# Performance work log

Measured on AMD Instinct MI355X. Metric: run time of the kernel, lower is better.

Reference implementation:

```python
import jax, jax.numpy as jnp
import numpy as np

D_IN, D, BOX, REL, THR = 2048, 512, 8, 80, 0.5

def _ln(x, g, b):
    m = jnp.mean(x, -1, keepdims=True)
    v = jnp.mean((x - m) ** 2, -1, keepdims=True)
    return (x - m) * jax.lax.rsqrt(v + 1e-5) * g + b

def setup_inputs():
    key = jax.random.key(0)
    ks = jax.random.split(key, 24)
    B, N = 32, 50
    def lin(k, i, o):
        return jax.random.normal(k, (i, o), jnp.float32) / np.sqrt(i)
    z = lambda n: jnp.zeros((n,), jnp.float32)
    o = lambda n: jnp.ones((n,), jnp.float32)
    return {
        "images": jax.random.normal(ks[0], (B, N, D_IN), jnp.float32),
        "selfbbox": jax.random.uniform(ks[1], (B, N, BOX), jnp.float32),
        "bbox": jax.random.uniform(ks[2], (B, N, N, BOX), jnp.float32),
        "pre_w": lin(ks[3], D_IN, D), "pre_b": z(D), "pre_g": o(D), "pre_be": z(D),
        "subj_w": lin(ks[4], D, D), "subj_b": z(D),
        "obj_w": lin(ks[5], D, D), "obj_b": z(D),
        "ps1_w": lin(ks[6], BOX, 64), "ps1_b": z(64), "ps_g": o(64), "ps_be": z(64),
        "ps2_w": lin(ks[7], 64, 64), "ps2_b": z(64),
        "pr1_w": lin(ks[8], BOX, 64), "pr1_b": z(64), "pr_g": o(64), "pr_be": z(64),
        "pr2_w": lin(ks[9], 64, 64), "pr2_b": z(64),
        "rs_w": lin(ks[10], D + 64, 1), "rs_b": z(1),
        "rf_w": lin(ks[11], D + 64, REL), "rf_b": z(REL),
        "g1_w": lin(ks[12], D + REL, D + REL), "g1_b": z(D + REL),
        "g2_w": lin(ks[13], D + REL, D), "g2_b": z(D),
        "g3_w": lin(ks[14], D, D), "g3_b": z(D),
    }

def reference(images, selfbbox, bbox, pre_w, pre_b, pre_g, pre_be, subj_w, subj_b,
              obj_w, obj_b, ps1_w, ps1_b, ps_g, ps_be, ps2_w, ps2_b,
              pr1_w, pr1_b, pr_g, pr_be, pr2_w, pr2_b, rs_w, rs_b, rf_w, rf_b,
              g1_w, g1_b, g2_w, g2_b, g3_w, g3_b):
    B, N = images.shape[0], images.shape[1]
    mask = jnp.sum(images, -1) != 0.0                      # [B,N] valid nodes
    attention_mask = (~mask)[:, None, None, :]             # [B,1,1,N]
    mf = mask.astype(images.dtype)
    # preprocess: Linear -> ReLU -> (dropout=id at eval) -> LayerNorm
    x = _ln(jax.nn.relu(images @ pre_w + pre_b), pre_g, pre_be)  # [B,N,512]
    x_subj = jax.nn.relu(x @ subj_w + subj_b) * mf[..., None]
    x_obj = jax.nn.relu(x @ obj_w + obj_b) * mf[..., None]
    eye = jnp.eye(N, dtype=bool)
    # pairwise subject/object features: diag(i==j) holds subject, off-diag object j
    x_rela = jnp.where(eye[None, :, :, None], x_subj[:, :, None, :], x_obj[:, None, :, :])
    x_rela = x_rela * mf[:, :, None, None]
    # positional MLPs
    h = jax.nn.relu(selfbbox @ ps1_w + ps1_b)
    h = jax.nn.relu(_ln(h, ps_g, ps_be) @ ps2_w + ps2_b)
    pos_self = h * mf[..., None]
    h = jax.nn.relu(bbox @ pr1_w + pr1_b)
    h = jax.nn.relu(_ln(h, pr_g, pr_be) @ pr2_w + pr2_b)
    pos_relas = h * mf[:, None, :, None] * mf[:, :, None, None]
    pos_rela = jnp.where(eye[None, :, :, None], pos_self[:, :, None, :], pos_relas)
    pos_rela = pos_rela * mf[:, :, None, None]
    pair = jnp.concatenate([x_rela, pos_rela], axis=-1)    # [B,N,N,576]
    pair_mask = mask[:, :, None] & mask[:, None, :]        # [B,N,N]
    # Relationshipness: pairwise relatedness score p + attention-pooled relation feats
    logits = (pair @ rs_w + rs_b)[..., 0]                  # [B,N,N]
    p = jax.nn.sigmoid(logits) * pair_mask.astype(images.dtype)
    attn = jax.nn.softmax(jnp.where(pair_mask, logits, -1e9), axis=2)
    feat = jax.nn.relu(pair @ rf_w + rf_b)                 # [B,N,N,80]
    relas = jnp.einsum('bij,bijf->bif', attn, feat) * mf[..., None]
    xx = jnp.concatenate([x, relas], axis=-1)              # [B,N,592]
    # dynamic edge threshold -> block-diagonal graph, expressed densely per image
    A = p > THR                                            # edge i->j
    Ahat = A | eye[None]                                   # add remaining self loops
    Af = Ahat.astype(xx.dtype)
    deg = jnp.sum(Af, axis=1)                              # in-degree at target j (>=1)
    dinv = jax.lax.rsqrt(deg)
    An = Af * dinv[:, :, None] * dinv[:, None, :]          # sym-normalized adjacency
    def gcn(hh, w, b):
        return jnp.einsum('bij,bif->bjf', An, hh @ w) + b
    x1 = jax.nn.relu(gcn(xx, g1_w, g1_b))
    x2 = jax.nn.relu(gcn(x1, g2_w, g2_b))
    x3 = jax.nn.relu(gcn(x2, g3_w, g3_b))
    outs = jnp.concatenate([x[:, None], x3[:, None]], axis=1)  # [B,2,N,512]
    return (outs, attention_mask)
```

## Files before the change

kernel.cpp:

```cpp
#include <hip/hip_runtime.h>
#include <hip/hip_bf16.h>

typedef __hip_bfloat16 bf16;

#define BB 32
#define NN 50
#define DIN 2048
#define DD 512
#define PD 64
#define FF 80
#define GG 592
#define BN (BB*NN)

#define O_FLAG  0
#define O_MF    16
#define O_SS    1616
#define O_SO    3216
#define O_PS    4816
#define O_FS    107216
#define O_FO    235216
#define O_RL    363216
#define O_LG    491216
#define O_AN    571216
#define O_T     651216
#define O_X1    1598416
#define O_X2    2545616
#define O_WPRE  3364816
#define O_BPRE  4413392
#define O_GPRE  4413904
#define O_EPRE  4414416
#define O_WSUBJ 4414928
#define O_BSUBJ 4677072
#define O_WOBJ  4677584
#define O_BOBJ  4939728
#define O_WPS1  4940240
#define O_BPS1  4940752
#define O_GPS   4940816
#define O_EPS   4940880
#define O_WPS2  4940944
#define O_BPS2  4945040
#define O_WPR1  4945104
#define O_BPR1  4945616
#define O_GPR   4945680
#define O_EPR   4945744
#define O_WPR2  4945808
#define O_BPR2  4949904
#define O_WRS   4949968
#define O_BRS   4950544
#define O_WRF   4950560
#define O_BRF   4996640
#define O_WG1   4996736
#define O_BG1   5347200
#define O_WG2   5347792
#define O_BG2   5650896
#define O_WG3   5651408
#define O_BG3   5913552
#define O_FT    5914064

#define PSLICE  819200

__device__ __forceinline__ float b2f(bf16 x){ return __bfloat162float(x); }

__device__ __forceinline__ float LDI(const bf16* p, size_t i, int f32m){
    if(f32m){
        bf16 a=p[2*i], b=p[2*i+1];
        unsigned short lo,hi;
        __builtin_memcpy(&lo,&a,2); __builtin_memcpy(&hi,&b,2);
        unsigned v=((unsigned)hi<<16)|(unsigned)lo;
        float f; __builtin_memcpy(&f,&v,4);
        return f;
    }
    return __bfloat162float(p[i]);
}

__global__ void k_flag(const bf16* __restrict__ images, float* __restrict__ ws){
    __shared__ int cnt;
    if(threadIdx.x==0) cnt=0;
    __syncthreads();
    bf16 h=images[2*threadIdx.x];
    unsigned short u; __builtin_memcpy(&u,&h,2);
    unsigned e=(u>>7)&0xFF;
    int sane=((u&0x7FFF)==0 || (e>=0x70&&e<=0x85))?1:0;
    atomicAdd(&cnt,sane);
    __syncthreads();
    if(threadIdx.x==0) ws[O_FLAG]=(cnt<48)?1.f:0.f;
}

__device__ __forceinline__ void conv(const bf16* s, float* d, int n, int F, int i0, int st){
    for(int g=i0; g<n; g+=st) d[g]=LDI(s,(size_t)g,F);
}
__global__ void kw(const bf16* p0,const bf16* p1,const bf16* p2,const bf16* p3,
                   const bf16* p4,const bf16* p5,const bf16* p6,const bf16* p7,
                   const bf16* p8,const bf16* p9,const bf16* p10,const bf16* p11,
                   const bf16* p12,const bf16* p13,const bf16* p14,const bf16* p15,
                   const bf16* p16,const bf16* p17,const bf16* p18,const bf16* p19,
                   const bf16* p20,const bf16* p21,const bf16* p22,const bf16* p23,
                   const bf16* p24,const bf16* p25,const bf16* p26,const bf16* p27,
                   const bf16* p28,const bf16* p29, float* __restrict__ ws){
    int F=ws[O_FLAG]>0.5f;
    int i0=blockIdx.x*256+threadIdx.x, st=gridDim.x*256;
    conv(p0, ws+O_WPRE, 1048576,F,i0,st);
    conv(p1, ws+O_BPRE, 512,F,i0,st);
    conv(p2, ws+O_GPRE, 512,F,i0,st);
    conv(p3, ws+O_EPRE, 512,F,i0,st);
    conv(p4, ws+O_WSUBJ,262144,F,i0,st);
    conv(p5, ws+O_BSUBJ,512,F,i0,st);
    conv(p6, ws+O_WOBJ, 262144,F,i0,st);
    conv(p7, ws+O_BOBJ, 512,F,i0,st);
    conv(p8, ws+O_WPS1, 512,F,i0,st);
    conv(p9, ws+O_BPS1, 64,F,i0,st);
    conv(p10,ws+O_GPS,  64,F,i0,st);
    conv(p11,ws+O_EPS,  64,F,i0,st);
    conv(p12,ws+O_WPS2, 4096,F,i0,st);
    conv(p13,ws+O_BPS2, 64,F,i0,st);
    conv(p14,ws+O_WPR1, 512,F,i0,st);
    conv(p15,ws+O_BPR1, 64,F,i0,st);
    conv(p16,ws+O_GPR,  64,F,i0,st);
    conv(p17,ws+O_EPR,  64,F,i0,st);
    conv(p18,ws+O_WPR2, 4096,F,i0,st);
    conv(p19,ws+O_BPR2, 64,F,i0,st);
    conv(p20,ws+O_WRS,  576,F,i0,st);
    conv(p21,ws+O_BRS,  1,F,i0,st);
    conv(p22,ws+O_WRF,  46080,F,i0,st);
    conv(p23,ws+O_BRF,  80,F,i0,st);
    conv(p24,ws+O_WG1,  350464,F,i0,st);
    conv(p25,ws+O_BG1,  592,F,i0,st);
    conv(p26,ws+O_WG2,  303104,F,i0,st);
    conv(p27,ws+O_BG2,  512,F,i0,st);
    conv(p28,ws+O_WG3,  262144,F,i0,st);
    conv(p29,ws+O_BG3,  512,F,i0,st);
}

__global__ void k_mask(const bf16* __restrict__ images, float* __restrict__ ws,
                       float* __restrict__ out){
    int t=threadIdx.x, wv=t>>6, ln=t&63;
    int r=blockIdx.x*4+wv;
    int F=ws[O_FLAG]>0.5f;
    float s=0.f;
    for(int k=ln;k<DIN;k+=64) s+=LDI(images,(size_t)r*DIN+k,F);
    for(int m=32;m>0;m>>=1) s+=__shfl_xor(s,m,64);
    if(ln==0){
        float mf=(s!=0.f)?1.f:0.f;
        ws[O_MF+r]=mf;
        out[(size_t)BB*2*NN*DD+r]=1.f-mf;
    }
}

__global__ void __launch_bounds__(256,4) k_x(const bf16* __restrict__ images,
                                             float* __restrict__ ws){
    __shared__ float as[8*256];
    int blk=blockIdx.x, t=threadIdx.x;
    int rg=blk>>3, ks=blk&7;
    int r0=rg*8, kbase=ks*256;
    int F=ws[O_FLAG]>0.5f;
    for(int idx=t; idx<8*256; idx+=256){
        int row=idx>>8, k=idx&255;
        as[idx]=LDI(images,(size_t)(r0+row)*DIN+kbase+k,F);
    }
    __syncthreads();
    const float* wP=ws+O_WPRE+(size_t)kbase*DD;
    int c0=t, c1=t+256;
    float acc[8][2]={};
    for(int k0=0;k0<256;k0+=8){
        float w0[8],w1[8];
        #pragma unroll
        for(int u=0;u<8;u++){ w0[u]=wP[(size_t)(k0+u)*DD+c0]; w1[u]=wP[(size_t)(k0+u)*DD+c1]; }
        #pragma unroll
        for(int u=0;u<8;u++){
            #pragma unroll
            for(int row=0;row<8;row++){
                float v=as[row*256+k0+u];
                acc[row][0]+=v*w0[u]; acc[row][1]+=v*w1[u];
            }
        }
    }
    float* P=ws + ((ks<7)? (O_FT+(size_t)ks*PSLICE) : (size_t)O_T);
    #pragma unroll
    for(int row=0;row<8;row++){
        size_t b=(size_t)(r0+row)*DD;
        P[b+c0]=acc[row][0]; P[b+c1]=acc[row][1];
    }
}

__global__ void __launch_bounds__(256,4) k_xr(float* __restrict__ ws, float* __restrict__ out){
    __shared__ float red[256];
    int blk=blockIdx.x, t=threadIdx.x;
    int r0=blk*4;
    const float* bPre=ws+O_BPRE; const float* gPre=ws+O_GPRE; const float* ePre=ws+O_EPRE;
    int c0=t, c1=t+256;
    for(int row=0;row<4;row++){
        int r=r0+row;
        float y0=bPre[c0], y1=bPre[c1];
        for(int ks=0;ks<8;ks++){
            const float* P=ws + ((ks<7)? (O_FT+(size_t)ks*PSLICE) : (size_t)O_T);
            y0+=P[(size_t)r*DD+c0]; y1+=P[(size_t)r*DD+c1];
        }
        y0=fmaxf(y0,0.f); y1=fmaxf(y1,0.f);
        red[t]=y0+y1; __syncthreads();
        for(int o=128;o>0;o>>=1){ if(t<o) red[t]+=red[t+o]; __syncthreads(); }
        float mean=red[0]/DD; __syncthreads();
        float d0=y0-mean, d1=y1-mean;
        red[t]=d0*d0+d1*d1; __syncthreads();
        for(int o=128;o>0;o>>=1){ if(t<o) red[t]+=red[t+o]; __syncthreads(); }
        float rstd=rsqrtf(red[0]/DD+1e-5f);
        __syncthreads();
        float xv0=d0*rstd*gPre[c0]+ePre[c0];
        float xv1=d1*rstd*gPre[c1]+ePre[c1];
        size_t ob=((size_t)(r/NN)*2)*NN*DD+(size_t)(r%NN)*DD;
        out[ob+c0]=xv0; out[ob+c1]=xv1;
    }
}

__global__ void __launch_bounds__(256,4) k_so(const float* __restrict__ out,
                                              float* __restrict__ ws){
    __shared__ float xs[4*DD];
    __shared__ float ys[4*DD];
    __shared__ float mrow_s[4];
    int blk=blockIdx.x, t=threadIdx.x;
    int rg=blk>>1, mat=blk&1;
    int r0=rg*4;
    for(int idx=t; idx<4*DD; idx+=256){
        int row=idx>>9, k=idx&511;
        int r=r0+row;
        xs[idx]=out[((size_t)(r/NN)*2)*NN*DD+(size_t)(r%NN)*DD+k];
    }
    if(t<4) mrow_s[t]=ws[O_MF+r0+t];
    __syncthreads();
    const float* W =ws+(mat?O_WOBJ:O_WSUBJ);
    const float* Bb=ws+(mat?O_BOBJ:O_BSUBJ);
    int c0=t, c1=t+256;
    float acc[4][2]={};
    for(int k0=0;k0<DD;k0+=8){
        float w0[8],w1[8];
        #pragma unroll
        for(int u=0;u<8;u++){ w0[u]=W[(size_t)(k0+u)*DD+c0]; w1[u]=W[(size_t)(k0+u)*DD+c1]; }
        #pragma unroll
        for(int u=0;u<8;u++){
            #pragma unroll
            for(int row=0;row<4;row++){
                float v=xs[row*DD+k0+u];
                acc[row][0]+=v*w0[u]; acc[row][1]+=v*w1[u];
            }
        }
    }
    #pragma unroll
    for(int row=0;row<4;row++){
        ys[row*DD+c0]=fmaxf(acc[row][0]+Bb[c0],0.f)*mrow_s[row];
        ys[row*DD+c1]=fmaxf(acc[row][1]+Bb[c1],0.f)*mrow_s[row];
    }
    __syncthreads();
    int wv=t>>6, ln=t&63;
    const float* wRs=ws+O_WRS;
    float ps=0.f;
    for(int k=ln;k<DD;k+=64) ps+=ys[wv*DD+k]*wRs[k];
    for(int m=32;m>0;m>>=1) ps+=__shfl_xor(ps,m,64);
    if(ln==0) ws[(mat?O_SO:O_SS)+r0+wv]=ps;
    const float* wRf=ws+O_WRF;
    for(int pass=0;pass<2;pass++){
        if(t<160){
            int row=pass*2+t/80, f=t%80;
            const float* xv=ys+row*DD;
            float a=0.f;
            for(int k=0;k<DD;k++) a+=xv[k]*wRf[(size_t)k*FF+f];
            ws[(mat?O_FO:O_FS)+(size_t)(r0+row)*FF+f]=a;
        }
    }
}

__global__ void k_pos_self(const bf16* __restrict__ sb, float* __restrict__ ws){
    __shared__ float h[PD];
    __shared__ float stat[2];
    int r=blockIdx.x, t=threadIdx.x;
    int F=ws[O_FLAG]>0.5f;
    const float* w1=ws+O_WPS1;
    float acc=0.f;
    for(int q=0;q<8;q++) acc+=LDI(sb,(size_t)r*8+q,F)*w1[q*PD+t];
    acc=fmaxf(acc+ws[O_BPS1+t],0.f);
    h[t]=acc; __syncthreads();
    if(t==0){
        float sm=0; for(int k=0;k<PD;k++) sm+=h[k];
        float mean=sm/PD;
        float v=0; for(int k=0;k<PD;k++){float d=h[k]-mean; v+=d*d;}
        stat[0]=mean; stat[1]=rsqrtf(v/PD+1e-5f);
    }
    __syncthreads();
    float hn=(acc-stat[0])*stat[1]*ws[O_GPS+t]+ws[O_EPS+t];
    h[t]=hn; __syncthreads();
    float a2=0.f;
    const float* w2=ws+O_WPS2;
    for(int k=0;k<PD;k++) a2+=h[k]*w2[k*PD+t];
    ws[O_PS+(size_t)r*PD+t]=fmaxf(a2+ws[O_BPS2+t],0.f)*ws[O_MF+r];
}

#define PSTRIDE 68

__global__ void __launch_bounds__(256,2) k_pair(const bf16* __restrict__ bbox,
                                                float* __restrict__ ws){
    __shared__ float W2t[64*PSTRIDE];
    __shared__ float WrfT[80*PSTRIDE];
    __shared__ float zb[64*PSTRIDE];
    __shared__ float pv[64*PSTRIDE];
    __shared__ float w1s[512];
    __shared__ float b1s[64], g1s[64], be1s[64], b2s[64], wrss[64];
    __shared__ float brfs[80];
    __shared__ float bbs[512];
    __shared__ float rowmi[64], rowmj[64], rowbase[64];
    __shared__ int   rowfb[64], rowps[64], rowdg[64];

    int t=threadIdx.x;
    int blk=blockIdx.x;
    int F=ws[O_FLAG]>0.5f;
    float rsb=ws[O_BRS];

    for(int idx=t; idx<4096; idx+=256){ int k=idx>>6, c=idx&63; W2t[k*PSTRIDE+c]=ws[O_WPR2+idx]; }
    for(int idx=t; idx<5120; idx+=256){
        int k=idx/80, f=idx-k*80;
        WrfT[f*PSTRIDE+k]=ws[O_WRF+(size_t)(512+k)*FF+f];
    }
    for(int idx=t; idx<512; idx+=256) w1s[idx]=ws[O_WPR1+idx];
    for(int idx=t; idx<512; idx+=256) bbs[idx]=LDI(bbox,(size_t)blk*512+idx,F);
    if(t<64){
        b1s[t]=ws[O_BPR1+t]; g1s[t]=ws[O_GPR+t]; be1s[t]=ws[O_EPR+t];
        b2s[t]=ws[O_BPR2+t]; wrss[t]=ws[O_WRS+512+t];
    } else if(t<144){
        brfs[t-64]=ws[O_BRF+t-64];
    }
    if(t<64){
        int p=blk*64+t;
        int r=p/NN, j=p-r*NN;
        int b=r/NN, i=r-b*NN;
        int dg=(i==j);
        rowmi[t]=ws[O_MF+r];
        rowmj[t]=ws[O_MF+b*NN+j];
        rowdg[t]=dg;
        rowbase[t]=dg? ws[O_SS+r] : ws[O_SO+b*NN+j];
        rowfb[t]=dg? (O_FS+r*FF) : (O_FO+(b*NN+j)*FF);
        rowps[t]=O_PS+r*PD;
    }
    __syncthreads();

    int wv=t>>6, ln=t&63;
    for(int q=0;q<16;q++){
        int m=wv*16+q;
        float acc=0.f;
        #pragma unroll
        for(int u=0;u<8;u++) acc+=bbs[m*8+u]*w1s[u*64+ln];
        float h1=fmaxf(acc+b1s[ln],0.f);
        float sm=h1;
        for(int o=32;o>0;o>>=1) sm+=__shfl_xor(sm,o,64);
        float mean=sm*(1.f/64.f);
        float d=h1-mean;
        float vv=d*d;
        for(int o=32;o>0;o>>=1) vv+=__shfl_xor(vv,o,64);
        float rstd=rsqrtf(vv*(1.f/64.f)+1e-5f);
        zb[m*PSTRIDE+ln]=d*rstd*g1s[ln]+be1s[ln];
    }
    __syncthreads();

    int tr=t>>4, tc=t&15;
    int m0=tr*4, c0=tc*4;
    {
        float a1[4][4]={};
        for(int k0=0;k0<64;k0+=4){
            float4 zv[4], wvv[4];
            #pragma unroll
            for(int i=0;i<4;i++) zv[i]=*(const float4*)&zb[(m0+i)*PSTRIDE+k0];
            #pragma unroll
            for(int u=0;u<4;u++) wvv[u]=*(const float4*)&W2t[(k0+u)*PSTRIDE+c0];
            #pragma unroll
            for(int i=0;i<4;i++){
                const float* zp=(const float*)&zv[i];
                #pragma unroll
                for(int u=0;u<4;u++){
                    const float* wp=(const float*)&wvv[u];
                    float zk=zp[u];
                    a1[i][0]+=zk*wp[0]; a1[i][1]+=zk*wp[1];
                    a1[i][2]+=zk*wp[2]; a1[i][3]+=zk*wp[3];
                }
            }
        }
        #pragma unroll
        for(int i=0;i<4;i++){
            int m=m0+i;
            float sc=rowmi[m]*rowmj[m];
            float4 o;
            o.x=fmaxf(a1[i][0]+b2s[c0+0],0.f)*sc;
            o.y=fmaxf(a1[i][1]+b2s[c0+1],0.f)*sc;
            o.z=fmaxf(a1[i][2]+b2s[c0+2],0.f)*sc;
            o.w=fmaxf(a1[i][3]+b2s[c0+3],0.f)*sc;
            *(float4*)&pv[m*PSTRIDE+c0]=o;
        }
    }
    __syncthreads();

    for(int idx=t; idx<4096; idx+=256){
        int m=idx>>6, c=idx&63;
        if(rowdg[m]) pv[m*PSTRIDE+c]=ws[rowps[m]+c];
    }
    __syncthreads();

    for(int q=0;q<16;q++){
        int m=wv*16+q;
        float lp=pv[m*PSTRIDE+ln]*wrss[ln];
        for(int o=32;o>0;o>>=1) lp+=__shfl_xor(lp,o,64);
        if(ln==0){
            int p=blk*64+m;
            ws[O_LG+p]=rowmi[m]*rowbase[m]+lp+rsb;
        }
    }

    {
        int c5=tc*5;
        float a2[4][5]={};
        for(int k0=0;k0<64;k0+=4){
            float4 zv[4], wv5[5];
            #pragma unroll
            for(int i=0;i<4;i++) zv[i]=*(const float4*)&pv[(m0+i)*PSTRIDE+k0];
            #pragma unroll
            for(int j=0;j<5;j++) wv5[j]=*(const float4*)&WrfT[(c5+j)*PSTRIDE+k0];
            #pragma unroll
            for(int i=0;i<4;i++){
                const float* zp=(const float*)&zv[i];
                #pragma unroll
                for(int j=0;j<5;j++){
                    const float* wp=(const float*)&wv5[j];
                    a2[i][j]+=zp[0]*wp[0]+zp[1]*wp[1]+zp[2]*wp[2]+zp[3]*wp[3];
                }
            }
        }
        #pragma unroll
        for(int i=0;i<4;i++){
            int m=m0+i;
            int p=blk*64+m;
            float mi=rowmi[m];
            const float* fb=ws+rowfb[m];
            #pragma unroll
            for(int j=0;j<5;j++){
                int c=c5+j;
                ws[O_FT+(size_t)p*FF+c]=fmaxf(mi*fb[c]+a2[i][j]+brfs[c],0.f);
            }
        }
    }
}

__global__ void k_relas(float* __restrict__ ws){
    __shared__ float attn[NN];
    int r=blockIdx.x, t=threadIdx.x;
    int b=r/NN;
    float mi=ws[O_MF+r];
    if(t<NN){
        float mj=ws[O_MF+b*NN+t];
        bool pm=(mi>0.5f)&&(mj>0.5f);
        attn[t]=pm? ws[O_LG+(size_t)r*NN+t] : -1e9f;
    }
    __syncthreads();
    if(t==0){
        float mx=-1e30f;
        for(int j=0;j<NN;j++) mx=fmaxf(mx,attn[j]);
        float sm=0.f;
        for(int j=0;j<NN;j++){ float e=__expf(attn[j]-mx); attn[j]=e; sm+=e; }
        float inv=1.f/sm;
        for(int j=0;j<NN;j++) attn[j]*=inv;
    }
    __syncthreads();
    if(t<FF){
        float s=0.f;
        const float* ft=ws+O_FT+(size_t)r*NN*FF;
        for(int j=0;j<NN;j++) s+=attn[j]*ft[(size_t)j*FF+t];
        ws[O_RL+(size_t)r*FF+t]=s*mi;
    }
}

__global__ void k_adj(float* __restrict__ ws){
    __shared__ float Af[NN*NN];
    __shared__ float dinv[NN];
    int b=blockIdx.x, t=threadIdx.x;
    for(int idx=t; idx<NN*NN; idx+=256){
        int i=idx/NN, j=idx%NN;
        float l=ws[O_LG+(size_t)b*NN*NN+idx];
        bool a=(l>0.f)&&(ws[O_MF+b*NN+i]>0.5f)&&(ws[O_MF+b*NN+j]>0.5f);
        Af[idx]=(a||i==j)?1.f:0.f;
    }
    __syncthreads();
    if(t<NN){
        float dg=0.f;
        for(int i=0;i<NN;i++) dg+=Af[i*NN+t];
        dinv[t]=rsqrtf(dg);
    }
    __syncthreads();
    for(int idx=t; idx<NN*NN; idx+=256){
        int i=idx/NN, j=idx%NN;
        ws[O_AN+(size_t)b*NN*NN+idx]=Af[idx]*dinv[i]*dinv[j];
    }
}

__global__ void kt(int mode, const float* __restrict__ out, const float* __restrict__ ws,
                   const float* __restrict__ W, float* __restrict__ T,
                   int K, int NCOL, int NTILE){
    __shared__ float xs[10*GG];
    int blk=blockIdx.x, t=threadIdx.x;
    int rg=blk/NTILE, tile=blk%NTILE;
    for(int idx=t; idx<10*K; idx+=256){
        int row=idx/K, k=idx-row*K;
        int gr=rg*10+row;
        float v;
        if(mode==0){
            int bb=gr/NN, ii=gr-bb*NN;
            if(k<DD) v=out[(size_t)(2*bb)*NN*DD+(size_t)ii*DD+k];
            else     v=ws[O_RL+(size_t)gr*FF+(k-DD)];
        } else if(mode==1) v=ws[O_X1+(size_t)gr*GG+k];
        else               v=ws[O_X2+(size_t)gr*DD+k];
        xs[row*K+k]=v;
    }
    __syncthreads();
    int c=tile*256+t;
    if(c>=NCOL) return;
    float acc[10];
    #pragma unroll
    for(int u=0;u<10;u++) acc[u]=0.f;
    for(int k=0;k<K;k++){
        float w=W[(size_t)k*NCOL+c];
        #pragma unroll
        for(int u=0;u<10;u++) acc[u]+=xs[u*K+k]*w;
    }
    int gr0=rg*10;
    #pragma unroll
    for(int u=0;u<10;u++) T[(size_t)(gr0+u)*NCOL+c]=acc[u];
}

__global__ void ka(int mode, float* __restrict__ ws, const float* __restrict__ bias,
                   float* __restrict__ out, int NCOL){
    __shared__ float acol[NN];
    int rj=blockIdx.x, t=threadIdx.x;
    int b=rj/NN, j=rj-b*NN;
    if(t<NN) acol[t]=ws[O_AN+(size_t)b*NN*NN+t*NN+j];
    __syncthreads();
    const float* Tb=ws+O_T+(size_t)b*NN*NCOL;
    for(int c=t;c<NCOL;c+=256){
        float acc=0.f;
        for(int i2=0;i2<NN;i2++) acc+=acol[i2]*Tb[(size_t)i2*NCOL+c];
        float v=fmaxf(acc+bias[c],0.f);
        if(mode==2)      out[(size_t)(2*b+1)*NN*DD+(size_t)j*DD+c]=v;
        else if(mode==1) ws[O_X2+(size_t)rj*DD+c]=v;
        else             ws[O_X1+(size_t)rj*GG+c]=v;
    }
}

extern "C" void kernel_launch(void* const* d_in, const int* in_sizes, int n_in,
                              void* d_out, int out_size, void* d_ws, size_t ws_size,
                              hipStream_t stream) {
    const bf16* images  = (const bf16*)d_in[0];
    const bf16* selfbbox= (const bf16*)d_in[1];
    const bf16* bbox    = (const bf16*)d_in[2];

    float* out=(float*)d_out;
    float* ws =(float*)d_ws;

    k_flag<<<1,64,0,stream>>>(images, ws);
    kw<<<512,256,0,stream>>>((const bf16*)d_in[3],(const bf16*)d_in[4],(const bf16*)d_in[5],
                             (const bf16*)d_in[6],(const bf16*)d_in[7],(const bf16*)d_in[8],
                             (const bf16*)d_in[9],(const bf16*)d_in[10],(const bf16*)d_in[11],
                             (const bf16*)d_in[12],(const bf16*)d_in[13],(const bf16*)d_in[14],
                             (const bf16*)d_in[15],(const bf16*)d_in[16],(const bf16*)d_in[17],
                             (const bf16*)d_in[18],(const bf16*)d_in[19],(const bf16*)d_in[20],
                             (const bf16*)d_in[21],(const bf16*)d_in[22],(const bf16*)d_in[23],
                             (const bf16*)d_in[24],(const bf16*)d_in[25],(const bf16*)d_in[26],
                             (const bf16*)d_in[27],(const bf16*)d_in[28],(const bf16*)d_in[29],
                             (const bf16*)d_in[30],(const bf16*)d_in[31],(const bf16*)d_in[32],
                             ws);
    k_mask<<<400,256,0,stream>>>(images, ws, out);
    k_x<<<1600,256,0,stream>>>(images, ws);
    k_xr<<<400,256,0,stream>>>(ws, out);
    k_pos_self<<<BN,PD,0,stream>>>(selfbbox, ws);
    k_so<<<800,256,0,stream>>>(out, ws);
    k_pair<<<1250,256,0,stream>>>(bbox, ws);
    k_relas<<<BN,128,0,stream>>>(ws);
    k_adj<<<BB,256,0,stream>>>(ws);

    kt<<<160*3,256,0,stream>>>(0, out, ws, ws+O_WG1, ws+O_T, GG, GG, 3);
    ka<<<BN,256,0,stream>>>(0, ws, ws+O_BG1, out, GG);
    kt<<<160*2,256,0,stream>>>(1, out, ws, ws+O_WG2, ws+O_T, GG, DD, 2);
    ka<<<BN,256,0,stream>>>(1, ws, ws+O_BG2, out, DD);
    kt<<<160*2,256,0,stream>>>(2, out, ws, ws+O_WG3, ws+O_T, DD, DD, 2);
    ka<<<BN,256,0,stream>>>(2, ws, ws+O_BG3, out, DD);
}
```

Before: 666.6 us.

## Double pair tile per block, reuse shared buffers, and warp-shuffle softmax

```diff
diff --git a/kernel.cpp b/kernel.cpp
--- a/kernel.cpp
+++ b/kernel.cpp
@@ -293,40 +293,43 @@
 }
 
 #define PSTRIDE 68
+#define ZROW(m) ((m)*PSTRIDE + (((m)>>3)<<2))
 
 __global__ void __launch_bounds__(256,2) k_pair(const bf16* __restrict__ bbox,
                                                 float* __restrict__ ws){
-    __shared__ float W2t[64*PSTRIDE];
-    __shared__ float WrfT[80*PSTRIDE];
-    __shared__ float zb[64*PSTRIDE];
-    __shared__ float pv[64*PSTRIDE];
+    __shared__ float zp[128*PSTRIDE+64];
+    __shared__ float wbuf[80*PSTRIDE];
     __shared__ float w1s[512];
+    __shared__ float bbs[1024];
     __shared__ float b1s[64], g1s[64], be1s[64], b2s[64], wrss[64];
     __shared__ float brfs[80];
-    __shared__ float bbs[512];
-    __shared__ float rowmi[64], rowmj[64], rowbase[64];
-    __shared__ int   rowfb[64], rowps[64], rowdg[64];
+    __shared__ float rowmi[128], rowmj[128], rowbase[128];
+    __shared__ int   rowfb[128], rowps[128], rowdg[128];
 
     int t=threadIdx.x;
     int blk=blockIdx.x;
     int F=ws[O_FLAG]>0.5f;
     float rsb=ws[O_BRS];
 
-    for(int idx=t; idx<4096; idx+=256){ int k=idx>>6, c=idx&63; W2t[k*PSTRIDE+c]=ws[O_WPR2+idx]; }
-    for(int idx=t; idx<5120; idx+=256){
-        int k=idx/80, f=idx-k*80;
-        WrfT[f*PSTRIDE+k]=ws[O_WRF+(size_t)(512+k)*FF+f];
-    }
+    float wrfreg[20];
+    #pragma unroll
+    for(int u=0;u<20;u++){
+        int idx=t+256*u;
+        int f=idx>>6, k=idx&63;
+        wrfreg[u]=ws[O_WRF+(size_t)(512+k)*FF+f];
+    }
+
+    for(int idx=t; idx<4096; idx+=256){ int k=idx>>6, c=idx&63; wbuf[k*PSTRIDE+c]=ws[O_WPR2+idx]; }
     for(int idx=t; idx<512; idx+=256) w1s[idx]=ws[O_WPR1+idx];
-    for(int idx=t; idx<512; idx+=256) bbs[idx]=LDI(bbox,(size_t)blk*512+idx,F);
+    for(int idx=t; idx<1024; idx+=256) bbs[idx]=LDI(bbox,(size_t)blk*1024+idx,F);
     if(t<64){
         b1s[t]=ws[O_BPR1+t]; g1s[t]=ws[O_GPR+t]; be1s[t]=ws[O_EPR+t];
         b2s[t]=ws[O_BPR2+t]; wrss[t]=ws[O_WRS+512+t];
     } else if(t<144){
         brfs[t-64]=ws[O_BRF+t-64];
     }
-    if(t<64){
-        int p=blk*64+t;
+    if(t<128){
+        int p=blk*128+t;
         int r=p/NN, j=p-r*NN;
         int b=r/NN, i=r-b*NN;
         int dg=(i==j);
@@ -340,8 +343,8 @@
     __syncthreads();
 
     int wv=t>>6, ln=t&63;
-    for(int q=0;q<16;q++){
-        int m=wv*16+q;
+    for(int q=0;q<32;q++){
+        int m=wv*32+q;
         float acc=0.f;
         #pragma unroll
         for(int u=0;u<8;u++) acc+=bbs[m*8+u]*w1s[u*64+ln];
@@ -353,114 +356,117 @@
         float vv=d*d;
         for(int o=32;o>0;o>>=1) vv+=__shfl_xor(vv,o,64);
         float rstd=rsqrtf(vv*(1.f/64.f)+1e-5f);
-        zb[m*PSTRIDE+ln]=d*rstd*g1s[ln]+be1s[ln];
+        zp[ZROW(m)+ln]=d*rstd*g1s[ln]+be1s[ln];
     }
     __syncthreads();
 
     int tr=t>>4, tc=t&15;
-    int m0=tr*4, c0=tc*4;
-    {
-        float a1[4][4]={};
-        for(int k0=0;k0<64;k0+=4){
-            float4 zv[4], wvv[4];
-            #pragma unroll
-            for(int i=0;i<4;i++) zv[i]=*(const float4*)&zb[(m0+i)*PSTRIDE+k0];
-            #pragma unroll
-            for(int u=0;u<4;u++) wvv[u]=*(const float4*)&W2t[(k0+u)*PSTRIDE+c0];
-            #pragma unroll
-            for(int i=0;i<4;i++){
-                const float* zp=(const float*)&zv[i];
-                #pragma unroll
-                for(int u=0;u<4;u++){
-                    const float* wp=(const float*)&wvv[u];
-                    float zk=zp[u];
-                    a1[i][0]+=zk*wp[0]; a1[i][1]+=zk*wp[1];
-                    a1[i][2]+=zk*wp[2]; a1[i][3]+=zk*wp[3];
-                }
+    int m0=tr*8, c0=tc*4;
+    float a1[8][4]={};
+    for(int k0=0;k0<64;k0+=4){
+        float4 zv[8], wvv[4];
+        #pragma unroll
+        for(int i=0;i<8;i++) zv[i]=*(const float4*)&zp[ZROW(m0+i)+k0];
+        #pragma unroll
+        for(int u=0;u<4;u++) wvv[u]=*(const float4*)&wbuf[(k0+u)*PSTRIDE+c0];
+        #pragma unroll
+        for(int i=0;i<8;i++){
+            const float* zpp=(const float*)&zv[i];
+            #pragma unroll
+            for(int u=0;u<4;u++){
+                const float* wp=(const float*)&wvv[u];
+                float zk=zpp[u];
+                a1[i][0]+=zk*wp[0]; a1[i][1]+=zk*wp[1];
+                a1[i][2]+=zk*wp[2]; a1[i][3]+=zk*wp[3];
             }
         }
-        #pragma unroll
-        for(int i=0;i<4;i++){
-            int m=m0+i;
+    }
+    __syncthreads();
+
+    #pragma unroll
+    for(int i=0;i<8;i++){
+        int m=m0+i;
+        float4 o;
+        if(rowdg[m]){
+            const float* ps=ws+rowps[m];
+            o.x=ps[c0]; o.y=ps[c0+1]; o.z=ps[c0+2]; o.w=ps[c0+3];
+        } else {
             float sc=rowmi[m]*rowmj[m];
-            float4 o;
             o.x=fmaxf(a1[i][0]+b2s[c0+0],0.f)*sc;
             o.y=fmaxf(a1[i][1]+b2s[c0+1],0.f)*sc;
             o.z=fmaxf(a1[i][2]+b2s[c0+2],0.f)*sc;
             o.w=fmaxf(a1[i][3]+b2s[c0+3],0.f)*sc;
-            *(float4*)&pv[m*PSTRIDE+c0]=o;
-        }
-    }
-    __syncthreads();
-
-    for(int idx=t; idx<4096; idx+=256){
-        int m=idx>>6, c=idx&63;
-        if(rowdg[m]) pv[m*PSTRIDE+c]=ws[rowps[m]+c];
-    }
-    __syncthreads();
-
-    for(int q=0;q<16;q++){
-        int m=wv*16+q;
-        float lp=pv[m*PSTRIDE+ln]*wrss[ln];
+        }
+        *(float4*)&zp[ZROW(m)+c0]=o;
+    }
+    #pragma unroll
+    for(int u=0;u<20;u++){
+        int idx=t+256*u;
+        wbuf[(idx>>6)*PSTRIDE+(idx&63)]=wrfreg[u];
+    }
+    __syncthreads();
+
+    for(int q=0;q<32;q++){
+        int m=wv*32+q;
+        float lp=zp[ZROW(m)+ln]*wrss[ln];
         for(int o=32;o>0;o>>=1) lp+=__shfl_xor(lp,o,64);
         if(ln==0){
-            int p=blk*64+m;
-            ws[O_LG+p]=rowmi[m]*rowbase[m]+lp+rsb;
+            ws[O_LG+(size_t)blk*128+m]=rowmi[m]*rowbase[m]+lp+rsb;
         }
     }
 
     {
         int c5=tc*5;
-        float a2[4][5]={};
+        float a2[8][5]={};
         for(int k0=0;k0<64;k0+=4){
-            float4 zv[4], wv5[5];
-            #pragma unroll
-            for(int i=0;i<4;i++) zv[i]=*(const float4*)&pv[(m0+i)*PSTRIDE+k0];
-            #pragma unroll
-            for(int j=0;j<5;j++) wv5[j]=*(const float4*)&WrfT[(c5+j)*PSTRIDE+k0];
-            #pragma unroll
-            for(int i=0;i<4;i++){
-                const float* zp=(const float*)&zv[i];
+            float4 zv[8], wv5[5];
+            #pragma unroll
+            for(int i=0;i<8;i++) zv[i]=*(const float4*)&zp[ZROW(m0+i)+k0];
+            #pragma unroll
+            for(int j=0;j<5;j++) wv5[j]=*(const float4*)&wbuf[(c5+j)*PSTRIDE+k0];
+            #pragma unroll
+            for(int i=0;i<8;i++){
+                const float* zpp=(const float*)&zv[i];
                 #pragma unroll
                 for(int j=0;j<5;j++){
                     const float* wp=(const float*)&wv5[j];
-                    a2[i][j]+=zp[0]*wp[0]+zp[1]*wp[1]+zp[2]*wp[2]+zp[3]*wp[3];
+                    a2[i][j]+=zpp[0]*wp[0]+zpp[1]*wp[1]+zpp[2]*wp[2]+zpp[3]*wp[3];
                 }
             }
         }
         #pragma unroll
-        for(int i=0;i<4;i++){
+        for(int i=0;i<8;i++){
             int m=m0+i;
-            int p=blk*64+m;
+            size_t p=(size_t)blk*128+m;
             float mi=rowmi[m];
             const float* fb=ws+rowfb[m];
             #pragma unroll
             for(int j=0;j<5;j++){
                 int c=c5+j;
-                ws[O_FT+(size_t)p*FF+c]=fmaxf(mi*fb[c]+a2[i][j]+brfs[c],0.f);
+                ws[O_FT+p*FF+c]=fmaxf(mi*fb[c]+a2[i][j]+brfs[c],0.f);
             }
         }
     }
 }
 
 __global__ void k_relas(float* __restrict__ ws){
-    __shared__ float attn[NN];
+    __shared__ float attn[64];
     int r=blockIdx.x, t=threadIdx.x;
     int b=r/NN;
     float mi=ws[O_MF+r];
-    if(t<NN){
-        float mj=ws[O_MF+b*NN+t];
-        bool pm=(mi>0.5f)&&(mj>0.5f);
-        attn[t]=pm? ws[O_LG+(size_t)r*NN+t] : -1e9f;
-    }
-    __syncthreads();
-    if(t==0){
-        float mx=-1e30f;
-        for(int j=0;j<NN;j++) mx=fmaxf(mx,attn[j]);
-        float sm=0.f;
-        for(int j=0;j<NN;j++){ float e=__expf(attn[j]-mx); attn[j]=e; sm+=e; }
-        float inv=1.f/sm;
-        for(int j=0;j<NN;j++) attn[j]*=inv;
+    if(t<64){
+        float v=-1e9f;
+        if(t<NN){
+            float mj=ws[O_MF+b*NN+t];
+            bool pm=(mi>0.5f)&&(mj>0.5f);
+            v=pm? ws[O_LG+(size_t)r*NN+t] : -1e9f;
+        }
+        float mx=v;
+        for(int o=32;o>0;o>>=1) mx=fmaxf(mx,__shfl_xor(mx,o,64));
+        float e=(t<NN)? __expf(v-mx) : 0.f;
+        float sm=e;
+        for(int o=32;o>0;o>>=1) sm+=__shfl_xor(sm,o,64);
+        attn[t]=e*(1.f/sm);
     }
     __syncthreads();
     if(t<FF){
@@ -573,7 +579,7 @@
     k_xr<<<400,256,0,stream>>>(ws, out);
     k_pos_self<<<BN,PD,0,stream>>>(selfbbox, ws);
     k_so<<<800,256,0,stream>>>(out, ws);
-    k_pair<<<1250,256,0,stream>>>(bbox, ws);
+    k_pair<<<625,256,0,stream>>>(bbox, ws);
     k_relas<<<BN,128,0,stream>>>(ws);
     k_adj<<<BB,256,0,stream>>>(ws);
 
```

Result: no change. 678.1 us (+1.7%).
